# Kernel optimization log

Hardware: AMD Instinct MI355X
Metric: run time of the kernel (lower is better)

## Reference

```python
import jax, jax.numpy as jnp
import numpy as np
import itertools

VOXEL_SIZE = np.array([0.05, 0.05, 0.1], np.float32)   # xyz, from cfg.voxel_size
GRID_OFFSET = np.array([0.0, -40.0, -3.0], np.float32)  # xyz, cfg.grid_bounds[:3]
BN_EPS = 1e-3

# ---------------- rulebook construction (numpy, mirrors spconv indice pairs) ----------------

def _enc(c, shape):
    Z, Y, X = shape
    c = c.astype(np.int64)
    return ((c[:, 0] * Z + c[:, 1]) * Y + c[:, 2]) * X + c[:, 3]

def _lookup(sk, order, q):
    pos = np.clip(np.searchsorted(sk, q), 0, len(sk) - 1)
    return np.where((q >= 0) & (sk[pos] == q), order[pos], -1).astype(np.int32)

def _subm_rulebook(coords, shape):
    # submanifold conv k=3, pad=1: output sites == input sites; neighbor = out + (k-1)
    keys = _enc(coords, shape)
    order = np.argsort(keys).astype(np.int32)
    sk = keys[order]
    dims = np.array(shape)
    rows = []
    for off in itertools.product((-1, 0, 1), repeat=3):
        nb = coords[:, 1:] + np.array(off)
        inb = ((nb >= 0) & (nb < dims)).all(1)
        full = np.concatenate([coords[:, :1], nb], 1)
        q = np.where(inb, _enc(full, shape), -1)
        rows.append(_lookup(sk, order, q))
    return np.stack(rows)  # [27, N] input index or -1

def _strided_rulebook(coords, shape_in, ksize, stride, pad):
    # regular sparse conv: out active = any site receiving a contribution; in = out*s - p + k
    ksize = np.array(ksize); stride = np.array(stride); pad = np.array(pad)
    shape_out = tuple((((np.array(shape_in) + 2 * pad - ksize) // stride) + 1).tolist())
    keys = _enc(coords, shape_in)
    order = np.argsort(keys).astype(np.int32)
    sk = keys[order]
    cand = []
    for k in itertools.product(*[range(int(x)) for x in ksize]):
        num = coords[:, 1:] + pad - np.array(k)
        ok = (num % stride == 0).all(1)
        o = num // stride
        ok &= (o >= 0).all(1) & (o < np.array(shape_out)).all(1)
        cand.append(np.concatenate([coords[ok, :1], o[ok]], 1))
    out_coords = np.unique(np.concatenate(cand, 0), axis=0).astype(np.int32)
    dims_in = np.array(shape_in)
    rows = []
    for k in itertools.product(*[range(int(x)) for x in ksize]):
        ic = out_coords[:, 1:] * stride - pad + np.array(k)
        inb = ((ic >= 0) & (ic < dims_in)).all(1)
        full = np.concatenate([out_coords[:, :1], ic], 1)
        q = np.where(inb, _enc(full, shape_in), -1)
        rows.append(_lookup(sk, order, q))
    return out_coords, np.stack(rows), shape_out

# ---------------- inputs ----------------

def setup_inputs() -> dict:
    rng = np.random.default_rng(0)
    B, NPB = 2, 8000
    shape0 = (41, 1600, 1280)
    parts = []
    for b in range(B):
        c = np.stack([rng.integers(0, shape0[0], 4 * NPB),
                      rng.integers(0, shape0[1], 4 * NPB),
                      rng.integers(0, shape0[2], 4 * NPB)], 1)
        c = np.unique(c, axis=0)[:NPB]
        parts.append(np.concatenate([np.full((len(c), 1), b), c], 1))
    coords0 = np.concatenate(parts, 0).astype(np.int32)

    rb0 = _subm_rulebook(coords0, shape0)
    coords1, rbc1, shape1 = _strided_rulebook(coords0, shape0, (3, 3, 3), (2, 2, 2), (1, 1, 1))
    rb1 = _subm_rulebook(coords1, shape1)
    coords2, rbc2, shape2 = _strided_rulebook(coords1, shape1, (3, 3, 3), (2, 2, 2), (1, 1, 1))
    rb2 = _subm_rulebook(coords2, shape2)
    coords3, rbc3, shape3 = _strided_rulebook(coords2, shape2, (3, 3, 3), (2, 2, 2), (0, 1, 1))
    rb3 = _subm_rulebook(coords3, shape3)
    coords4, rbc4, shape4 = _strided_rulebook(coords3, shape3, (3, 1, 1), (2, 1, 1), (0, 0, 0))

    def w(*s):
        return jnp.asarray((rng.standard_normal(s) * 0.1).astype(np.float32))

    inp = {"features": jnp.asarray(rng.standard_normal((len(coords0), 4)).astype(np.float32))}
    specs = [("1a", 27, 4, 16), ("1b", 27, 16, 16), ("1c", 27, 16, 32),
             ("2a", 27, 32, 32), ("2b", 27, 32, 32), ("2c", 27, 32, 64),
             ("3a", 27, 64, 64), ("3b", 27, 64, 64), ("3c", 27, 64, 64), ("3d", 27, 64, 64),
             ("4a", 27, 64, 64), ("4b", 27, 64, 64), ("4c", 27, 64, 64), ("4d", 3, 64, 64)]
    for name, K, ci, co in specs:
        inp["w" + name] = w(K, ci, co)
        inp["g" + name] = jnp.asarray((np.abs(rng.standard_normal(co)) + 0.5).astype(np.float32))
        inp["b" + name] = jnp.asarray((rng.standard_normal(co) * 0.1).astype(np.float32))
    inp.update(coordinates=jnp.asarray(coords0), coords1=jnp.asarray(coords1),
               coords2=jnp.asarray(coords2), coords3=jnp.asarray(coords3),
               rb0=jnp.asarray(rb0), rbc1=jnp.asarray(rbc1), rb1=jnp.asarray(rb1),
               rbc2=jnp.asarray(rbc2), rb2=jnp.asarray(rb2), rbc3=jnp.asarray(rbc3),
               rb3=jnp.asarray(rb3), rbc4=jnp.asarray(rbc4), batch_size=B)
    return inp

# ---------------- forward math ----------------

def _sconv(feat, rb, W):
    # gather-GEMM-scatter: rb[k,n] = input row feeding output n via kernel offset k (-1 = none)
    out = jnp.zeros((rb.shape[1], W.shape[2]), feat.dtype)
    for k in range(W.shape[0]):
        idx = rb[k]
        g = jnp.where(idx[:, None] >= 0, feat[jnp.clip(idx, 0)], 0.0)
        out = out + g @ W[k]
    return out

def _bn_relu(x, g, b):
    # BatchNorm1d in training mode over active voxels (biased var), eps=1e-3, then ReLU
    m = jnp.mean(x, 0)
    v = jnp.mean(jnp.square(x - m), 0)
    return jax.nn.relu((x - m) * (g / jnp.sqrt(v + BN_EPS)) + b)

def reference(features, w1a, g1a, b1a, w1b, g1b, b1b, w1c, g1c, b1c,
              w2a, g2a, b2a, w2b, g2b, b2b, w2c, g2c, b2c,
              w3a, g3a, b3a, w3b, g3b, b3b, w3c, g3c, b3c, w3d, g3d, b3d,
              w4a, g4a, b4a, w4b, g4b, b4b, w4c, g4c, b4c, w4d, g4d, b4d,
              coordinates, coords1, coords2, coords3,
              rb0, rbc1, rb1, rbc2, rb2, rbc3, rb3, rbc4, batch_size):
    f0 = features
    h = _bn_relu(_sconv(f0, rb0, w1a), g1a, b1a)
    h = _bn_relu(_sconv(h, rb0, w1b), g1b, b1b)
    f1 = _bn_relu(_sconv(h, rbc1, w1c), g1c, b1c)
    h = _bn_relu(_sconv(f1, rb1, w2a), g2a, b2a)
    h = _bn_relu(_sconv(h, rb1, w2b), g2b, b2b)
    f2 = _bn_relu(_sconv(h, rbc2, w2c), g2c, b2c)
    h = _bn_relu(_sconv(f2, rb2, w3a), g3a, b3a)
    h = _bn_relu(_sconv(h, rb2, w3b), g3b, b3b)
    h = _bn_relu(_sconv(h, rb2, w3c), g3c, b3c)
    f3 = _bn_relu(_sconv(h, rbc3, w3d), g3d, b3d)
    h = _bn_relu(_sconv(f3, rb3, w4a), g4a, b4a)
    h = _bn_relu(_sconv(h, rb3, w4b), g4b, b4b)
    h = _bn_relu(_sconv(h, rb3, w4c), g4c, b4c)
    f4 = _bn_relu(_sconv(h, rbc4, w4d), g4d, b4d)

    vs = jnp.asarray(VOXEL_SIZE)
    off = jnp.asarray(GRID_OFFSET)
    def to_global(stride, c):
        # indices are (b,z,y,x); flip -> (x,y,z,b); take xyz
        return jnp.flip(c, 1)[:, :3].astype(jnp.float32) * (vs * stride) + off
    xyz0 = to_global(1, coordinates)
    xyz1 = to_global(2, coords1)
    xyz2 = to_global(4, coords2)
    xyz3 = to_global(8, coords3)
    return (xyz0, f0, xyz1, f1, xyz2, f2, xyz3, f3, f4)
```

## Files before the change

### kernel.cpp

```cpp
#include <hip/hip_runtime.h>

#define BN_EPS 1e-3f
#define NREP 16

typedef __attribute__((ext_vector_type(8))) short short8;
typedef __attribute__((ext_vector_type(4))) float float4v;

__device__ __forceinline__ short f2bf(float f) {
    unsigned u = __float_as_uint(f);
    unsigned r = (u + 0x7FFFu + ((u >> 16) & 1u)) >> 16;
    return (short)r;
}

template <int N>
__device__ __forceinline__ void waitcnt_vm() {
    __builtin_amdgcn_s_waitcnt(0xF70 | (N & 15) | ((N >> 4) << 14));
}

__device__ __forceinline__ void wave_barrier() { asm volatile("s_barrier" ::: "memory"); }

__device__ __forceinline__ void dma16(const short* g, short* l) {
    __builtin_amdgcn_global_load_lds((const __attribute__((address_space(1))) void*)g,
                                     (__attribute__((address_space(3))) void*)l, 16, 0, 0);
}


__global__ __launch_bounds__(256) void zero_kernel(float* p, int n) {
    int i = blockIdx.x * 256 + threadIdx.x;
    if (i < n) p[i] = 0.f;
}

__global__ __launch_bounds__(256) void copy_kernel(const float* __restrict__ in,
                                                   float* __restrict__ out, int n) {
    int i = blockIdx.x * 256 + threadIdx.x;
    if (i < n) out[i] = in[i];
}

__global__ __launch_bounds__(256) void zero_rows_kernel(short* a, short* b, long maxN) {
    int t = threadIdx.x;
    if (t < 32) a[maxN * 32 + t] = 0;
    else if (t < 96) a[maxN * 64 + (t - 32)] = 0;
    else if (t < 128) b[maxN * 32 + (t - 96)] = 0;
    else if (t < 192) b[maxN * 64 + (t - 128)] = 0;
}

__global__ __launch_bounds__(256) void xyz_kernel(const int* __restrict__ coords,
                                                  float* __restrict__ out, int N,
                                                  float sx, float sy, float sz) {
    int n = blockIdx.x * 256 + threadIdx.x;
    if (n >= N) return;
    int4 c = ((const int4*)coords)[n];
    out[n * 3 + 0] = c.w * sx;
    out[n * 3 + 1] = c.z * sy - 40.0f;
    out[n * 3 + 2] = c.y * sz - 3.0f;
}

__global__ __launch_bounds__(256) void convert_f0(const float* __restrict__ f,
                                                  short* __restrict__ dst, int N) {
    int i = blockIdx.x * 256 + threadIdx.x;
    if (i >= N * 32) return;
    int c = i & 31, n = i >> 5;
    dst[i] = (c < 4) ? f2bf(f[n * 4 + c]) : (short)0;
}

struct PrepAll {
    const float* src[14];
    short* dst[14];
    int CI[14];
    int CO[14];
    int CHP[14];
    int cum[15];
};

__global__ __launch_bounds__(256) void prep_all_kernel(PrepAll d) {
    int i = blockIdx.x * 256 + threadIdx.x;
    if (i >= d.cum[14]) return;
    int l = 0;
    while (l < 13 && i >= d.cum[l + 1]) ++l;
    int f = i - d.cum[l];
    int CO = d.CO[l], CI = d.CI[l];
    int NCH = d.CHP[l] / 32, CT = CO / 16;
    int e = f & 7;
    int u = f >> 3;
    int l16 = u & 15;
    int q = (u >> 4) & 3;
    int u2 = u >> 6;
    int t = u2 % CT;
    int c = (u2 / CT) % NCH;
    int k = u2 / (CT * NCH);
    int ci = c * 32 + q * 8 + e;
    int co = t * 16 + l16;
    float v = (ci < CI) ? d.src[l][((size_t)k * CI + ci) * CO + co] : 0.f;
    d.dst[l][f] = f2bf(v);
}

struct ASet {
    short8 v0, v1, v2, v3;
};

template <int CHP, int CO, int K>
__global__ __launch_bounds__(256, 4) void sconv_hyb(const short* __restrict__ feat,
                                                    const int* __restrict__ rb,
                                                    const short* __restrict__ Wt,
                                                    float* __restrict__ out,
                                                    float* __restrict__ stats, int N, int zrow) {
    constexpr int NCH = CHP / 32;
    constexpr int CT = CO / 16;
    constexpr int BTILE = CO * CHP;
    constexpr int NB = BTILE / 512;
    constexpr int A = 2 * NCH;
    constexpr int ROWS = 128;

    __shared__ __align__(16) short ldsB[3 * BTILE];

    const int tid = threadIdx.x;
    const int w = tid >> 6;
    const int lane = tid & 63;
    const int quad = lane >> 4;
    const int l16 = lane & 15;
    const int m0 = blockIdx.x * ROWS;

    const short* fquad = feat + quad * 8;

    const int r0 = m0 + (w << 5) + l16;
    const int r1 = r0 + 16;
    const bool v0 = r0 < N;
    const bool v1 = r1 < N;
    const int* p0 = rb + (v0 ? r0 : 0);
    const int* p1 = rb + (v1 ? r1 : 0);

    auto loadRb = [&](int k) {
        int2 j;
        j.x = p0[(size_t)k * N];
        j.y = p1[(size_t)k * N];
        if (!v0) j.x = -1;
        if (!v1) j.y = -1;
        return j;
    };
    auto aliveOf = [&](int2 j) {
        return (__ballot(j.x >= 0) | __ballot(j.y >= 0)) != 0ull;
    };
    auto issueB = [&](int kp, int slot) {
        const short* wk = Wt + (size_t)kp * BTILE + lane * 8;
        short* bb = ldsB + slot * BTILE;
#pragma unroll
        for (int jj = 0; jj < (NB + 3) / 4; ++jj) {
            int j = jj * 4 + w;
            if (j < NB) dma16(wk + j * 512, bb + j * 512);
        }
    };
    auto issueA = [&](int2 j) {
        ASet s;
        const short* q0 = fquad + (size_t)(j.x < 0 ? zrow : j.x) * CHP;
        const short* q1 = fquad + (size_t)(j.y < 0 ? zrow : j.y) * CHP;
        s.v0 = *(const short8*)q0;
        s.v2 = *(const short8*)q1;
        if constexpr (NCH == 2) {
            s.v1 = *(const short8*)(q0 + 32);
            s.v3 = *(const short8*)(q1 + 32);
        } else {
            s.v1 = (short8)0;
            s.v3 = (short8)0;
        }
        return s;
    };

    float4v acc[2][CT];
#pragma unroll
    for (int mt = 0; mt < 2; ++mt)
#pragma unroll
        for (int t = 0; t < CT; ++t) acc[mt][t] = (float4v)0.f;

    constexpr int BW0 = NB / 4 + ((NB % 4) > 0 ? 1 : 0);
    constexpr int BW1 = NB / 4 + ((NB % 4) > 1 ? 1 : 0);
    constexpr int BW2 = NB / 4 + ((NB % 4) > 2 ? 1 : 0);
    constexpr int BW3 = NB / 4;

    int2 t0 = loadRb(0);
    int2 t1 = loadRb(1);
    waitcnt_vm<0>();
    bool alA = aliveOf(t0);
    bool alB = aliveOf(t1);
    int2 qA, qB, qC;
    qA.x = qA.y = qB.x = qB.y = qC.x = qC.y = -1;
    issueB(0, 0);
    if (K > 2) qA = loadRb(2);
    ASet sA = issueA(t0);
    issueB(1, 1);
    if (K > 3) qB = loadRb(3);
    ASet sB = issueA(t1);
    ASet sC;
    bool alC = false;

    int slotRd = 0, slotWr = 2;
#pragma unroll 1
    for (int i = 0; i < K; ++i) {
        if (i < K - 3) {
            if (w == 0) waitcnt_vm<BW0 + 2 + A>();
            else if (w == 1) waitcnt_vm<BW1 + 2 + A>();
            else if (w == 2) waitcnt_vm<BW2 + 2 + A>();
            else waitcnt_vm<BW3 + 2 + A>();
        } else if (i < K - 1) {
            if (w == 0) waitcnt_vm<BW0 + A>();
            else if (w == 1) waitcnt_vm<BW1 + A>();
            else if (w == 2) waitcnt_vm<BW2 + A>();
            else waitcnt_vm<BW3 + A>();
        } else {
            waitcnt_vm<0>();
        }
        __builtin_amdgcn_sched_barrier(0);
        wave_barrier();
        if (i + 2 < K) {
            issueB(i + 2, slotWr);
            if (i + 4 < K) qC = loadRb(i + 4);
            alC = aliveOf(qA);
            sC = issueA(qA);
        }
        if (alA) {
            const short* bb = ldsB + slotRd * BTILE;
#pragma unroll
            for (int c = 0; c < NCH; ++c) {
#pragma unroll
                for (int t = 0; t < CT; ++t) {
                    short8 bf = *(const short8*)(bb + ((c * CT + t) * 64 + quad * 16 + l16) * 8);
#pragma unroll
                    for (int mt = 0; mt < 2; ++mt) {
                        short8 af = (mt == 0) ? ((c == 0) ? sA.v0 : sA.v1)
                                              : ((c == 0) ? sA.v2 : sA.v3);
                        acc[mt][t] =
                            __builtin_amdgcn_mfma_f32_16x16x32_bf16(af, bf, acc[mt][t], 0, 0, 0);
                    }
                }
            }
        }
        sA = sB;
        sB = sC;
        alA = alB;
        alB = alC;
        qA = qB;
        qB = qC;
        slotRd = (slotRd == 2) ? 0 : slotRd + 1;
        slotWr = (slotWr == 2) ? 0 : slotWr + 1;
    }

#pragma unroll
    for (int mt = 0; mt < 2; ++mt)
#pragma unroll
        for (int t = 0; t < CT; ++t) {
            int col = t * 16 + l16;
#pragma unroll
            for (int r = 0; r < 4; ++r) {
                int orow = m0 + w * 32 + mt * 16 + quad * 4 + r;
                if (orow < N) out[(size_t)orow * CO + col] = acc[mt][t][r];
            }
        }

    __syncthreads();
    float* red = (float*)ldsB;
#pragma unroll
    for (int t = 0; t < CT; ++t) {
        float s = 0.f, ss = 0.f;
#pragma unroll
        for (int mt = 0; mt < 2; ++mt)
#pragma unroll
            for (int r = 0; r < 4; ++r) {
                float v = acc[mt][t][r];
                s += v;
                ss += v * v;
            }
        s += __shfl_xor(s, 16);
        s += __shfl_xor(s, 32);
        ss += __shfl_xor(ss, 16);
        ss += __shfl_xor(ss, 32);
        if (lane < 16) {
            red[w * 2 * CO + t * 16 + lane] = s;
            red[w * 2 * CO + CO + t * 16 + lane] = ss;
        }
    }
    __syncthreads();
    if (tid < 2 * CO) {
        float v = red[tid] + red[2 * CO + tid] + red[4 * CO + tid] + red[6 * CO + tid];
        float* st = stats + (size_t)(blockIdx.x & (NREP - 1)) * 128;
        atomicAdd(&st[(tid < CO) ? tid : (64 + tid - CO)], v);
    }
}

template <int COUT, int CHPN, bool F32OUT, bool BFOUT>
__global__ __launch_bounds__(256) void bn_apply(const float* __restrict__ x,
                                                const float* __restrict__ stats,
                                                const float* __restrict__ g,
                                                const float* __restrict__ b,
                                                float* __restrict__ fout,
                                                short* __restrict__ bfout, int N) {
    constexpr int CW = BFOUT ? CHPN : COUT;
    constexpr int CV = CW / 8;
    __shared__ float ssc[COUT];
    __shared__ float ssh[COUT];
    int tid = threadIdx.x;
    if (tid < COUT) {
        float s = 0.f, q = 0.f;
#pragma unroll
        for (int r = 0; r < NREP; ++r) {
            s += stats[r * 128 + tid];
            q += stats[r * 128 + 64 + tid];
        }
        float inv = 1.0f / (float)N;
        float m = s * inv;
        float v = q * inv - m * m;
        float sc = g[tid] / sqrtf(v + BN_EPS);
        ssc[tid] = sc;
        ssh[tid] = b[tid] - m * sc;
    }
    __syncthreads();
    long i = (long)blockIdx.x * 256 + tid;
    if (i >= (long)N * CV) return;
    int c8 = (int)(i % CV);
    long n = i / CV;
    int cb = c8 * 8;
    float y[8];
#pragma unroll
    for (int j = 0; j < 8; ++j) y[j] = 0.f;
    if (cb < COUT) {
        const float4v* xr = (const float4v*)(x + n * COUT + cb);
        float4v a0 = xr[0];
        float4v a1 = xr[1];
#pragma unroll
        for (int j = 0; j < 4; ++j) {
            y[j] = fmaxf(a0[j] * ssc[cb + j] + ssh[cb + j], 0.f);
            y[4 + j] = fmaxf(a1[j] * ssc[cb + 4 + j] + ssh[cb + 4 + j], 0.f);
        }
        if constexpr (F32OUT) {
            float* fo = fout + n * COUT + cb;
            if ((((unsigned long long)fout) & 15ull) == 0) {
                float4v o0, o1;
#pragma unroll
                for (int j = 0; j < 4; ++j) {
                    o0[j] = y[j];
                    o1[j] = y[4 + j];
                }
                ((float4v*)fo)[0] = o0;
                ((float4v*)fo)[1] = o1;
            } else {
#pragma unroll
                for (int j = 0; j < 8; ++j) fo[j] = y[j];
            }
        }
    }
    if constexpr (BFOUT) {
        short8 p;
#pragma unroll
        for (int j = 0; j < 8; ++j) p[j] = f2bf(y[j]);
        *(short8*)(bfout + n * CHPN + cb) = p;
    }
}


template <int CHP, int CO, int K>
static void conv(const short* fin, const int* rb, const short* wt, float* preact, float* stats,
                 int N, int zrow, hipStream_t stream) {
    dim3 grid((N + 127) / 128);
    hipLaunchKernelGGL((sconv_hyb<CHP, CO, K>), grid, dim3(256), 0, stream, fin, rb, wt, preact,
                       stats, N, zrow);
}

template <int COUT, int CHPN, bool F32OUT, bool BFOUT>
static void apply(const float* preact, const float* stats, const float* g, const float* b,
                  float* fout, short* bfout, int N, hipStream_t stream) {
    constexpr int CW = BFOUT ? CHPN : COUT;
    constexpr int CV = CW / 8;
    int blocks = (int)(((long)N * CV + 255) / 256);
    hipLaunchKernelGGL((bn_apply<COUT, CHPN, F32OUT, BFOUT>), dim3(blocks), dim3(256), 0, stream,
                       preact, stats, g, b, fout, bfout, N);
}

extern "C" void kernel_launch(void* const* d_in, const int* in_sizes, int n_in, void* d_out,
                              int out_size, void* d_ws, size_t ws_size, hipStream_t stream) {
    const float* features = (const float*)d_in[0];
    const float* W[14];
    const float* G[14];
    const float* Bb[14];
    for (int i = 0; i < 14; ++i) {
        W[i] = (const float*)d_in[1 + 3 * i];
        G[i] = (const float*)d_in[2 + 3 * i];
        Bb[i] = (const float*)d_in[3 + 3 * i];
    }
    const int* coords0 = (const int*)d_in[43];
    const int* coords1 = (const int*)d_in[44];
    const int* coords2 = (const int*)d_in[45];
    const int* coords3 = (const int*)d_in[46];
    const int* rb0 = (const int*)d_in[47];
    const int* rbc1 = (const int*)d_in[48];
    const int* rb1 = (const int*)d_in[49];
    const int* rbc2 = (const int*)d_in[50];
    const int* rb2 = (const int*)d_in[51];
    const int* rbc3 = (const int*)d_in[52];
    const int* rb3 = (const int*)d_in[53];
    const int* rbc4 = (const int*)d_in[54];

    const int N0 = in_sizes[0] / 4;
    const int N1 = in_sizes[44] / 4;
    const int N2 = in_sizes[45] / 4;
    const int N3 = in_sizes[46] / 4;
    const int N4 = in_sizes[54] / 3;

    float* out = (float*)d_out;
    long off = 0;
    float* xyz0 = out + off; off += (long)N0 * 3;
    float* f0   = out + off; off += (long)N0 * 4;
    float* xyz1 = out + off; off += (long)N1 * 3;
    float* f1   = out + off; off += (long)N1 * 32;
    float* xyz2 = out + off; off += (long)N2 * 3;
    float* f2   = out + off; off += (long)N2 * 64;
    float* xyz3 = out + off; off += (long)N3 * 3;
    float* f3   = out + off; off += (long)N3 * 64;
    float* f4   = out + off;

    long maxN = N0;
    if (N1 > maxN) maxN = N1;
    if (N2 > maxN) maxN = N2;
    if (N3 > maxN) maxN = N3;
    if (N4 > maxN) maxN = N4;
    const int zrow = (int)maxN;

    float* preact = (float*)d_ws;
    float* statsBase = preact + (size_t)maxN * 64;
    short* bfA = (short*)(statsBase + 14 * NREP * 128);
    short* bfB = bfA + (size_t)(maxN + 1) * 64;
    short* wtBase = bfB + (size_t)(maxN + 1) * 64;

    static const int KK[14] = {27, 27, 27, 27, 27, 27, 27, 27, 27, 27, 27, 27, 27, 3};
    static const int CI[14] = {4, 16, 16, 32, 32, 32, 64, 64, 64, 64, 64, 64, 64, 64};
    static const int CO[14] = {16, 16, 32, 32, 32, 64, 64, 64, 64, 64, 64, 64, 64, 64};
    short* WT[14];
    PrepAll pd;
    {
        size_t o = 0;
        int cum = 0;
        for (int l = 0; l < 14; ++l) {
            WT[l] = wtBase + o;
            int chp = CI[l] <= 32 ? 32 : 64;
            pd.src[l] = W[l];
            pd.dst[l] = WT[l];
            pd.CI[l] = CI[l];
            pd.CO[l] = CO[l];
            pd.CHP[l] = chp;
            pd.cum[l] = cum;
            cum += KK[l] * CO[l] * chp;
            o += (size_t)KK[l] * CO[l] * chp;
        }
        pd.cum[14] = cum;
    }

    int nstats = 14 * NREP * 128;
    hipLaunchKernelGGL(zero_kernel, dim3((nstats + 255) / 256), dim3(256), 0, stream, statsBase,
                       nstats);
    hipLaunchKernelGGL(zero_rows_kernel, dim3(1), dim3(256), 0, stream, bfA, bfB, maxN);
    hipLaunchKernelGGL(prep_all_kernel, dim3((pd.cum[14] + 255) / 256), dim3(256), 0, stream, pd);

    hipLaunchKernelGGL(copy_kernel, dim3((N0 * 4 + 255) / 256), dim3(256), 0, stream, features, f0,
                       N0 * 4);
    hipLaunchKernelGGL(xyz_kernel, dim3((N0 + 255) / 256), dim3(256), 0, stream, coords0, xyz0, N0,
                       0.05f, 0.05f, 0.1f);
    hipLaunchKernelGGL(xyz_kernel, dim3((N1 + 255) / 256), dim3(256), 0, stream, coords1, xyz1, N1,
                       0.1f, 0.1f, 0.2f);
    hipLaunchKernelGGL(xyz_kernel, dim3((N2 + 255) / 256), dim3(256), 0, stream, coords2, xyz2, N2,
                       0.2f, 0.2f, 0.4f);
    hipLaunchKernelGGL(xyz_kernel, dim3((N3 + 255) / 256), dim3(256), 0, stream, coords3, xyz3, N3,
                       0.4f, 0.4f, 0.8f);
    hipLaunchKernelGGL(convert_f0, dim3((N0 * 32 + 255) / 256), dim3(256), 0, stream, features,
                       bfA, N0);

    float* st = statsBase;
#define STAT(l) (st + (size_t)(l)*NREP * 128)

    conv<32, 16, 27>(bfA, rb0, WT[0], preact, STAT(0), N0, zrow, stream);
    apply<16, 32, false, true>(preact, STAT(0), G[0], Bb[0], nullptr, bfB, N0, stream);
    conv<32, 16, 27>(bfB, rb0, WT[1], preact, STAT(1), N0, zrow, stream);
    apply<16, 32, false, true>(preact, STAT(1), G[1], Bb[1], nullptr, bfA, N0, stream);
    conv<32, 32, 27>(bfA, rbc1, WT[2], preact, STAT(2), N1, zrow, stream);
    apply<32, 32, true, true>(preact, STAT(2), G[2], Bb[2], f1, bfB, N1, stream);

    conv<32, 32, 27>(bfB, rb1, WT[3], preact, STAT(3), N1, zrow, stream);
    apply<32, 32, false, true>(preact, STAT(3), G[3], Bb[3], nullptr, bfA, N1, stream);
    conv<32, 32, 27>(bfA, rb1, WT[4], preact, STAT(4), N1, zrow, stream);
    apply<32, 32, false, true>(preact, STAT(4), G[4], Bb[4], nullptr, bfB, N1, stream);
    conv<32, 64, 27>(bfB, rbc2, WT[5], preact, STAT(5), N2, zrow, stream);
    apply<64, 64, true, true>(preact, STAT(5), G[5], Bb[5], f2, bfA, N2, stream);

    conv<64, 64, 27>(bfA, rb2, WT[6], preact, STAT(6), N2, zrow, stream);
    apply<64, 64, false, true>(preact, STAT(6), G[6], Bb[6], nullptr, bfB, N2, stream);
    conv<64, 64, 27>(bfB, rb2, WT[7], preact, STAT(7), N2, zrow, stream);
    apply<64, 64, false, true>(preact, STAT(7), G[7], Bb[7], nullptr, bfA, N2, stream);
    conv<64, 64, 27>(bfA, rb2, WT[8], preact, STAT(8), N2, zrow, stream);
    apply<64, 64, false, true>(preact, STAT(8), G[8], Bb[8], nullptr, bfB, N2, stream);
    conv<64, 64, 27>(bfB, rbc3, WT[9], preact, STAT(9), N3, zrow, stream);
    apply<64, 64, true, true>(preact, STAT(9), G[9], Bb[9], f3, bfA, N3, stream);

    conv<64, 64, 27>(bfA, rb3, WT[10], preact, STAT(10), N3, zrow, stream);
    apply<64, 64, false, true>(preact, STAT(10), G[10], Bb[10], nullptr, bfB, N3, stream);
    conv<64, 64, 27>(bfB, rb3, WT[11], preact, STAT(11), N3, zrow, stream);
    apply<64, 64, false, true>(preact, STAT(11), G[11], Bb[11], nullptr, bfA, N3, stream);
    conv<64, 64, 27>(bfA, rb3, WT[12], preact, STAT(12), N3, zrow, stream);
    apply<64, 64, false, true>(preact, STAT(12), G[12], Bb[12], nullptr, bfB, N3, stream);
    conv<64, 64, 3>(bfB, rbc4, WT[13], preact, STAT(13), N4, zrow, stream);
    apply<64, 64, true, false>(preact, STAT(13), G[13], Bb[13], f4, nullptr, N4, stream);
#undef STAT
}
```

Measured before the change: 706.6 us.

## Replace LDS-staged block conv with single-wave blocks loading weights into registers

The sparse conv kernel moves from 256-thread blocks that staged weight tiles into a triple-buffered LDS ring via DMA and barriers to 64-thread single-wave blocks of 32 rows. Each wave loads its weight fragments straight from global memory into registers every kernel offset, which removes the LDS staging, the per-wave waitcnt bookkeeping and the block barriers. The statistics reduction now does per-wave atomics instead of an LDS cross-wave reduction. In exchange, weight reuse across waves is lost, so global and L2 weight traffic grows about four-fold, there are four times as many stats atomics, and the weight loads are not prefetched ahead of the MFMAs.

```diff
diff --git a/kernel.cpp b/kernel.cpp
--- a/kernel.cpp
+++ b/kernel.cpp
@@ -15,13 +15,6 @@
 template <int N>
 __device__ __forceinline__ void waitcnt_vm() {
     __builtin_amdgcn_s_waitcnt(0xF70 | (N & 15) | ((N >> 4) << 14));
-}
-
-__device__ __forceinline__ void wave_barrier() { asm volatile("s_barrier" ::: "memory"); }
-
-__device__ __forceinline__ void dma16(const short* g, short* l) {
-    __builtin_amdgcn_global_load_lds((const __attribute__((address_space(1))) void*)g,
-                                     (__attribute__((address_space(3))) void*)l, 16, 0, 0);
 }
 
 
@@ -99,30 +92,24 @@
 };
 
 template <int CHP, int CO, int K>
-__global__ __launch_bounds__(256, 4) void sconv_hyb(const short* __restrict__ feat,
-                                                    const int* __restrict__ rb,
-                                                    const short* __restrict__ Wt,
-                                                    float* __restrict__ out,
-                                                    float* __restrict__ stats, int N, int zrow) {
+__global__ __launch_bounds__(64, 3) void sconv_wav(const short* __restrict__ feat,
+                                                   const int* __restrict__ rb,
+                                                   const short* __restrict__ Wt,
+                                                   float* __restrict__ out,
+                                                   float* __restrict__ stats, int N, int zrow) {
     constexpr int NCH = CHP / 32;
     constexpr int CT = CO / 16;
     constexpr int BTILE = CO * CHP;
-    constexpr int NB = BTILE / 512;
-    constexpr int A = 2 * NCH;
-    constexpr int ROWS = 128;
-
-    __shared__ __align__(16) short ldsB[3 * BTILE];
-
-    const int tid = threadIdx.x;
-    const int w = tid >> 6;
-    const int lane = tid & 63;
+    constexpr int BF = NCH * CT;
+
+    const int lane = threadIdx.x & 63;
     const int quad = lane >> 4;
     const int l16 = lane & 15;
-    const int m0 = blockIdx.x * ROWS;
+    const int m0 = blockIdx.x * 32;
 
     const short* fquad = feat + quad * 8;
 
-    const int r0 = m0 + (w << 5) + l16;
+    const int r0 = m0 + l16;
     const int r1 = r0 + 16;
     const bool v0 = r0 < N;
     const bool v1 = r1 < N;
@@ -140,14 +127,17 @@
     auto aliveOf = [&](int2 j) {
         return (__ballot(j.x >= 0) | __ballot(j.y >= 0)) != 0ull;
     };
-    auto issueB = [&](int kp, int slot) {
-        const short* wk = Wt + (size_t)kp * BTILE + lane * 8;
-        short* bb = ldsB + slot * BTILE;
-#pragma unroll
-        for (int jj = 0; jj < (NB + 3) / 4; ++jj) {
-            int j = jj * 4 + w;
-            if (j < NB) dma16(wk + j * 512, bb + j * 512);
-        }
+
+    struct BSet {
+        short8 f[BF];
+    };
+    auto loadB = [&](int k) {
+        BSet b;
+        const short* wk = Wt + (size_t)k * BTILE;
+#pragma unroll
+        for (int j = 0; j < BF; ++j)
+            b.f[j] = *(const short8*)(wk + ((j * 64) + quad * 16 + l16) * 8);
+        return b;
     };
     auto issueA = [&](int2 j) {
         ASet s;
@@ -171,11 +161,6 @@
 #pragma unroll
         for (int t = 0; t < CT; ++t) acc[mt][t] = (float4v)0.f;
 
-    constexpr int BW0 = NB / 4 + ((NB % 4) > 0 ? 1 : 0);
-    constexpr int BW1 = NB / 4 + ((NB % 4) > 1 ? 1 : 0);
-    constexpr int BW2 = NB / 4 + ((NB % 4) > 2 ? 1 : 0);
-    constexpr int BW3 = NB / 4;
-
     int2 t0 = loadRb(0);
     int2 t1 = loadRb(1);
     waitcnt_vm<0>();
@@ -183,46 +168,30 @@
     bool alB = aliveOf(t1);
     int2 qA, qB, qC;
     qA.x = qA.y = qB.x = qB.y = qC.x = qC.y = -1;
-    issueB(0, 0);
     if (K > 2) qA = loadRb(2);
+    if (K > 3) qB = loadRb(3);
     ASet sA = issueA(t0);
-    issueB(1, 1);
-    if (K > 3) qB = loadRb(3);
     ASet sB = issueA(t1);
     ASet sC;
     bool alC = false;
 
-    int slotRd = 0, slotWr = 2;
 #pragma unroll 1
     for (int i = 0; i < K; ++i) {
-        if (i < K - 3) {
-            if (w == 0) waitcnt_vm<BW0 + 2 + A>();
-            else if (w == 1) waitcnt_vm<BW1 + 2 + A>();
-            else if (w == 2) waitcnt_vm<BW2 + 2 + A>();
-            else waitcnt_vm<BW3 + 2 + A>();
-        } else if (i < K - 1) {
-            if (w == 0) waitcnt_vm<BW0 + A>();
-            else if (w == 1) waitcnt_vm<BW1 + A>();
-            else if (w == 2) waitcnt_vm<BW2 + A>();
-            else waitcnt_vm<BW3 + A>();
-        } else {
-            waitcnt_vm<0>();
-        }
-        __builtin_amdgcn_sched_barrier(0);
-        wave_barrier();
+        BSet bCur = loadB(i);
+        const bool haveRb = (i + 4 < K);
+        if (haveRb) qC = loadRb(i + 4);
+        if (haveRb) waitcnt_vm<2>();
+        else waitcnt_vm<0>();
         if (i + 2 < K) {
-            issueB(i + 2, slotWr);
-            if (i + 4 < K) qC = loadRb(i + 4);
             alC = aliveOf(qA);
             sC = issueA(qA);
         }
         if (alA) {
-            const short* bb = ldsB + slotRd * BTILE;
 #pragma unroll
             for (int c = 0; c < NCH; ++c) {
 #pragma unroll
                 for (int t = 0; t < CT; ++t) {
-                    short8 bf = *(const short8*)(bb + ((c * CT + t) * 64 + quad * 16 + l16) * 8);
+                    short8 bf = bCur.f[c * CT + t];
 #pragma unroll
                     for (int mt = 0; mt < 2; ++mt) {
                         short8 af = (mt == 0) ? ((c == 0) ? sA.v0 : sA.v1)
@@ -239,8 +208,6 @@
         alB = alC;
         qA = qB;
         qB = qC;
-        slotRd = (slotRd == 2) ? 0 : slotRd + 1;
-        slotWr = (slotWr == 2) ? 0 : slotWr + 1;
     }
 
 #pragma unroll
@@ -250,13 +217,12 @@
             int col = t * 16 + l16;
 #pragma unroll
             for (int r = 0; r < 4; ++r) {
-                int orow = m0 + w * 32 + mt * 16 + quad * 4 + r;
+                int orow = m0 + mt * 16 + quad * 4 + r;
                 if (orow < N) out[(size_t)orow * CO + col] = acc[mt][t][r];
             }
         }
 
-    __syncthreads();
-    float* red = (float*)ldsB;
+    float* st = stats + (size_t)(blockIdx.x & (NREP - 1)) * 128;
 #pragma unroll
     for (int t = 0; t < CT; ++t) {
         float s = 0.f, ss = 0.f;
@@ -273,15 +239,9 @@
         ss += __shfl_xor(ss, 16);
         ss += __shfl_xor(ss, 32);
         if (lane < 16) {
-            red[w * 2 * CO + t * 16 + lane] = s;
-            red[w * 2 * CO + CO + t * 16 + lane] = ss;
-        }
-    }
-    __syncthreads();
-    if (tid < 2 * CO) {
-        float v = red[tid] + red[2 * CO + tid] + red[4 * CO + tid] + red[6 * CO + tid];
-        float* st = stats + (size_t)(blockIdx.x & (NREP - 1)) * 128;
-        atomicAdd(&st[(tid < CO) ? tid : (64 + tid - CO)], v);
+            atomicAdd(&st[t * 16 + lane], s);
+            atomicAdd(&st[64 + t * 16 + lane], ss);
+        }
     }
 }
 
@@ -358,8 +318,8 @@
 template <int CHP, int CO, int K>
 static void conv(const short* fin, const int* rb, const short* wt, float* preact, float* stats,
                  int N, int zrow, hipStream_t stream) {
-    dim3 grid((N + 127) / 128);
-    hipLaunchKernelGGL((sconv_hyb<CHP, CO, K>), grid, dim3(256), 0, stream, fin, rb, wt, preact,
+    dim3 grid((N + 31) / 32);
+    hipLaunchKernelGGL((sconv_wav<CHP, CO, K>), grid, dim3(64), 0, stream, fin, rb, wt, preact,
                        stats, N, zrow);
 }
 
```

Measured after the change: 688.2 us. 1.03x faster.
